# Kernel optimization log

Measured on AMD Instinct MI355X. Metric: run time of the kernel, lower is better.

The kernel has to match this reference:

```python
import jax, jax.numpy as jnp
import numpy as np

B, N_H, N_W, DIM, HEADS = 2, 64, 64, 768, 12
HINT = 1024
HIDDEN = DIM * 2       # LTRM expand_ratio = 2
K_ECA = 5              # ECA kernel for C=768: int(|log2(768)/2 + 0.5|)=5 (odd)
TH_LO, TH_HI, MIN_EDGE = 0.02, 0.98, 64


def setup_inputs() -> dict:
    key = jax.random.key(0)
    ks = jax.random.split(key, 12)
    N = N_H * N_W
    x = jax.random.normal(ks[0], (B, N, DIM), jnp.float32)
    # alpha hint: left half = uniform noise (uncertain -> edge tokens),
    # right half = binary blocks aligned to the 16px token cells (easy tokens)
    blocks = (jax.random.uniform(ks[1], (B, 1, N_H, N_W)) > 0.5).astype(jnp.float32)
    blocks_up = jnp.repeat(jnp.repeat(blocks, HINT // N_H, axis=2), HINT // N_W, axis=3)
    noise = jax.random.uniform(ks[2], (B, 1, HINT, HINT))
    col = jnp.arange(HINT)[None, None, None, :]
    alpha_hint = jnp.where(col < HINT // 2, noise, blocks_up)
    s = 0.02
    return {
        "x": x,
        "alpha_hint": alpha_hint,
        # global attention (Hiera-style patched MaskUnitAttention, q_stride=1)
        "qkv_w": jax.random.normal(ks[3], (DIM, 3 * DIM), jnp.float32) * s,
        "qkv_b": jnp.zeros((3 * DIM,), jnp.float32),
        "proj_w": jax.random.normal(ks[4], (DIM, DIM), jnp.float32) * s,
        "proj_b": jnp.zeros((DIM,), jnp.float32),
        # LTRM
        "ln_g": jnp.ones((DIM,), jnp.float32),
        "ln_b": jnp.zeros((DIM,), jnp.float32),
        "fc1_w": jax.random.normal(ks[5], (DIM, HIDDEN), jnp.float32) * s,
        "fc1_b": jnp.zeros((HIDDEN,), jnp.float32),
        "fc2_w": jax.random.normal(ks[6], (HIDDEN, DIM), jnp.float32) * s,  # zeros in ckpt; random for non-trivial math
        "fc2_b": jnp.zeros((DIM,), jnp.float32),
        "eca_w": jax.random.normal(ks[7], (K_ECA,), jnp.float32) * 0.2,
    }


def _edge_mask(alpha_hint):
    # F.interpolate(mode='area') with exact integer factor == block mean
    Bn = alpha_hint.shape[0]
    f_h, f_w = HINT // N_H, HINT // N_W
    hint = alpha_hint.reshape(Bn, N_H, f_h, N_W, f_w).mean(axis=(2, 4)).reshape(Bn, N_H * N_W)
    edge = (hint > TH_LO) & (hint < TH_HI)
    # per-batch fallback: too few edge tokens -> route everything to attention
    edge = jnp.where(edge.sum(axis=1, keepdims=True) < MIN_EDGE, True, edge)
    return edge  # [B, N] bool


def _layernorm(h, g, b, eps=1e-5):
    mu = h.mean(-1, keepdims=True)
    var = ((h - mu) ** 2).mean(-1, keepdims=True)
    return (h - mu) * jax.lax.rsqrt(var + eps) * g + b


def reference(x, alpha_hint, qkv_w, qkv_b, proj_w, proj_b,
              ln_g, ln_b, fc1_w, fc1_b, fc2_w, fc2_b, eca_w):
    Bn, N, C = x.shape
    hd = C // HEADS
    edge = _edge_mask(alpha_hint)                      # [B, N] bool

    # ---- edge path: global SDPA restricted to edge tokens (masked form of
    # the gather->attend->scatter routing: same math, edge keys only) ----
    qkv = (x @ qkv_w + qkv_b).reshape(Bn, N, 3, HEADS, hd)
    q = qkv[:, :, 0].transpose(0, 2, 1, 3)             # [B,H,N,hd]
    k = qkv[:, :, 1].transpose(0, 2, 1, 3)
    v = qkv[:, :, 2].transpose(0, 2, 1, 3)
    scores = jnp.einsum('bhqd,bhkd->bhqk', q, k) / jnp.sqrt(jnp.asarray(hd, x.dtype))
    scores = scores + jnp.where(edge[:, None, None, :], 0.0, -1e9).astype(x.dtype)
    attn = jax.nn.softmax(scores, axis=-1)
    o = jnp.einsum('bhqk,bhkd->bhqd', attn, v)
    o = o.transpose(0, 2, 1, 3).reshape(Bn, N, C)
    attn_out = x + (o @ proj_w + proj_b)               # residual around attention

    # ---- easy path: LTRM (subset of tokens -> DWConv branch skipped,
    # exactly as in LTRM.forward when N != H*W) ----
    h = _layernorm(x, ln_g, ln_b)
    h = jax.nn.gelu(h @ fc1_w + fc1_b, approximate=False)
    h = jax.nn.gelu(h, approximate=False)
    h = h @ fc2_w + fc2_b                              # [B,N,C]
    # ECA: avg-pool over the routed (easy) token set -> masked mean
    easy = ~edge
    cnt = jnp.maximum(easy.sum(axis=1).astype(x.dtype), 1.0)      # [B]
    pooled = (h * easy[..., None]).sum(axis=1) / cnt[:, None]     # [B,C]
    g = jax.lax.conv_general_dilated(
        pooled[:, None, :], eca_w.reshape(1, 1, K_ECA), (1,), 'SAME',
        dimension_numbers=('NCH', 'OIH', 'NCH'))[:, 0, :]          # [B,C]
    h = h * jax.nn.sigmoid(g)[:, None, :]
    ltrm_out = x + h

    # ---- scatter-combine ----
    return jnp.where(edge[..., None], attn_out, ltrm_out)
```

## Files before the change

kernel.cpp:

```cpp
#include <hip/hip_runtime.h>

using u16 = unsigned short;
using short8 = __attribute__((ext_vector_type(8))) short;
using f32x4 = __attribute__((ext_vector_type(4))) float;

#define NTOK 4096
#define CDIM 768
#define QKVD 2304
#define NHEAD 12
#define NSPLIT 4
#define SCALE2 0.18033688011112042f
#define THRRAW 44.3614195558f

__device__ __forceinline__ u16 f2bf(float f) {
  unsigned u = __float_as_uint(f);
  u += 0x7FFFu + ((u >> 16) & 1u);
  return (u16)(u >> 16);
}
__device__ __forceinline__ float bf2f(u16 v) {
  return __uint_as_float(((unsigned)v) << 16);
}
__device__ __forceinline__ float fast_exp2(float x) {
  float r;
  asm("v_exp_f32 %0, %1" : "=v"(r) : "v"(x));
  return r;
}
__device__ __forceinline__ unsigned cvtpk(float lo, float hi) {
  unsigned r;
  asm("v_cvt_pk_bf16_f32 %0, %1, %2" : "=v"(r) : "v"(lo), "v"(hi));
  return r;
}

__device__ __forceinline__ void gload_lds16(const void* g, void* l) {
  __builtin_amdgcn_global_load_lds(
      (__attribute__((address_space(1))) void*)g,
      (__attribute__((address_space(3))) void*)l, 16u, 0, 0u);
}

__device__ __forceinline__ float gelu_exact(float z) {
  return 0.5f * z * (1.0f + erff(z * 0.70710678118654752f));
}

__global__ __launch_bounds__(256) void pool_hint_kernel(
    const float* __restrict__ ah, float* __restrict__ hint)
{
  const int bid = blockIdx.x;
  const int b = bid >> 6, cr = bid & 63;
  const int t = threadIdx.x;
  const float* base = ah + ((size_t)b * 1024 + (size_t)cr * 16) * 1024;
  float s = 0.f;
#pragma unroll
  for (int pr = 0; pr < 16; ++pr) {
    float4 v = *(const float4*)(base + (size_t)pr * 1024 + t * 4);
    s += v.x + v.y + v.z + v.w;
  }
  s += __shfl_xor(s, 1);
  s += __shfl_xor(s, 2);
  if ((t & 3) == 0)
    hint[b * NTOK + cr * 64 + (t >> 2)] = s * (1.f / 256.f);
}

__global__ __launch_bounds__(1024) void finalize_edge_kernel(
    const float* __restrict__ hint, int* __restrict__ edge,
    int* __restrict__ qidx, int* __restrict__ eidx,
    int* __restrict__ cntE, int* __restrict__ cntZ)
{
  const int b = blockIdx.x, t = threadIdx.x;
  __shared__ int wsum[16];
  __shared__ int scntE, scntZ, stot;
  int bits[4]; int s = 0;
#pragma unroll
  for (int j = 0; j < 4; ++j) {
    float h = hint[b * NTOK + t * 4 + j];
    bits[j] = (h > 0.02f && h < 0.98f) ? 1 : 0;
    s += bits[j];
    qidx[b * NTOK + t * 4 + j] = -1;
    eidx[b * NTOK + t * 4 + j] = -1;
  }
  int sw = s;
#pragma unroll
  for (int d = 1; d < 64; d <<= 1) sw += __shfl_xor(sw, d);
  const int l = t & 63, w = t >> 6;
  if (l == 0) wsum[w] = sw;
  if (t == 0) { scntE = 0; scntZ = 0; }
  __syncthreads();
  if (t == 0) { int a = 0; for (int i = 0; i < 16; ++i) a += wsum[i]; stot = a; }
  __syncthreads();
  const bool fb = stot < 64;
#pragma unroll
  for (int j = 0; j < 4; ++j) {
    int e = fb ? 1 : bits[j];
    edge[b * NTOK + t * 4 + j] = e;
    if (e) {
      int p = atomicAdd(&scntE, 1);
      qidx[b * NTOK + p] = t * 4 + j;
    } else {
      int p = atomicAdd(&scntZ, 1);
      eidx[b * NTOK + p] = t * 4 + j;
    }
  }
  __syncthreads();
  if (t == 0) { cntE[b] = scntE; cntZ[b] = scntZ; }
}

__global__ __launch_bounds__(256) void ln_kernel(
    const float* __restrict__ x, const float* __restrict__ gam,
    const float* __restrict__ bet, u16* __restrict__ lnb, u16* __restrict__ xb)
{
  const int row = blockIdx.x, t = threadIdx.x;
  const float* xr = x + (size_t)row * CDIM;
  float v[3];
#pragma unroll
  for (int j = 0; j < 3; ++j) v[j] = xr[t + j * 256];
  float s = v[0] + v[1] + v[2];
  float ss = v[0] * v[0] + v[1] * v[1] + v[2] * v[2];
#pragma unroll
  for (int d = 1; d < 64; d <<= 1) { s += __shfl_xor(s, d); ss += __shfl_xor(ss, d); }
  __shared__ float red[8];
  const int l = t & 63, w = t >> 6;
  if (l == 0) { red[w * 2] = s; red[w * 2 + 1] = ss; }
  __syncthreads();
  s = red[0] + red[2] + red[4] + red[6];
  ss = red[1] + red[3] + red[5] + red[7];
  const float mu = s * (1.f / 768.f);
  const float rstd = rsqrtf(ss * (1.f / 768.f) - mu * mu + 1e-5f);
#pragma unroll
  for (int j = 0; j < 3; ++j) {
    const int cc = t + j * 256;
    lnb[(size_t)row * CDIM + cc] = f2bf((v[j] - mu) * rstd * gam[cc] + bet[cc]);
    xb[(size_t)row * CDIM + cc] = f2bf(v[j]);
  }
}

__global__ __launch_bounds__(256) void transpose_all_kernel(
    const float* __restrict__ qkv_w, const float* __restrict__ proj_w,
    const float* __restrict__ fc1_w, const float* __restrict__ fc2_w,
    u16* __restrict__ qkvT, u16* __restrict__ projT,
    u16* __restrict__ fc1T, u16* __restrict__ fc2T)
{
  __shared__ float tile[32][33];
  int bid = blockIdx.x;
  const float* in; u16* outp; int K, N, bx, by;
  if (bid < 1728)      { in = qkv_w;  outp = qkvT; K = 768;  N = 2304; bx = bid % 72; by = bid / 72; }
  else if (bid < 2304) { bid -= 1728; in = proj_w; outp = projT; K = 768;  N = 768;  bx = bid % 24; by = bid / 24; }
  else if (bid < 3456) { bid -= 2304; in = fc1_w;  outp = fc1T; K = 768;  N = 1536; bx = bid % 48; by = bid / 48; }
  else                 { bid -= 3456; in = fc2_w;  outp = fc2T; K = 1536; N = 768;  bx = bid % 24; by = bid / 24; }
  const int tx = threadIdx.x & 31, ty = threadIdx.x >> 5;
#pragma unroll
  for (int j = 0; j < 32; j += 8)
    tile[ty + j][tx] = in[(size_t)(by * 32 + ty + j) * N + bx * 32 + tx];
  __syncthreads();
#pragma unroll
  for (int j = 0; j < 32; j += 8)
    outp[(size_t)(bx * 32 + ty + j) * K + by * 32 + tx] = f2bf(tile[tx][ty + j]);
}

template <int EPI, bool GATHER_A, bool SCATTER_OUT>
__global__ __launch_bounds__(256) void gemm_bt(
    const u16* __restrict__ A, const u16* __restrict__ Bt,
    const float* __restrict__ bias, const float* __restrict__ resid,
    const int* __restrict__ list, void* __restrict__ outp, int N, int K)
{
  const int bm = blockIdx.x, bn = blockIdx.y;
  const int b = bm >> 5, bmi = bm & 31;
  const int rb = bmi * 128;
  if (list[b * NTOK + rb] < 0) return;

  __shared__ __align__(16) u16 lA[128 * 32];
  __shared__ __align__(16) u16 lB[128 * 32];
  const int t = threadIdx.x;
  const int l = t & 63, w = t >> 6;
  const int g = l >> 4, c = l & 15;
  const int wr = w >> 1, wc = w & 1;

  f32x4 acc[4][4];
#pragma unroll
  for (int i = 0; i < 4; ++i)
#pragma unroll
    for (int j = 0; j < 4; ++j) acc[i][j] = f32x4{0.f, 0.f, 0.f, 0.f};

  const int srow = t >> 2;
  const int sslot = (t & 3) ^ (srow & 3);
  int ta0, ta1;
  if constexpr (GATHER_A) {
    ta0 = list[b * NTOK + rb + srow];       if (ta0 < 0) ta0 = 0;
    ta1 = list[b * NTOK + rb + 64 + srow];  if (ta1 < 0) ta1 = 0;
  } else {
    ta0 = rb + srow;
    ta1 = rb + 64 + srow;
  }
  const u16* gA0 = A + ((size_t)b * NTOK + ta0) * K + sslot * 8;
  const u16* gA1 = A + ((size_t)b * NTOK + ta1) * K + sslot * 8;
  const u16* gB0 = Bt + (size_t)(bn * 128 + srow) * K + sslot * 8;
  const u16* gB1 = Bt + (size_t)(bn * 128 + 64 + srow) * K + sslot * 8;
  char* ldA = (char*)lA + w * 1024;
  char* ldB = (char*)lB + w * 1024;

  for (int k0 = 0; k0 < K; k0 += 32) {
    __syncthreads();
    gload_lds16(gA0 + k0, ldA);
    gload_lds16(gA1 + k0, ldA + 4096);
    gload_lds16(gB0 + k0, ldB);
    gload_lds16(gB1 + k0, ldB + 4096);
    __syncthreads();
    short8 af[4], bfr[4];
#pragma unroll
    for (int mi = 0; mi < 4; ++mi) {
      int row = wr * 64 + mi * 16 + c;
      af[mi] = *(const short8*)((const char*)lA + row * 64 + ((g ^ (row & 3)) << 4));
    }
#pragma unroll
    for (int ni = 0; ni < 4; ++ni) {
      int row = wc * 64 + ni * 16 + c;
      bfr[ni] = *(const short8*)((const char*)lB + row * 64 + ((g ^ (row & 3)) << 4));
    }
#pragma unroll
    for (int mi = 0; mi < 4; ++mi)
#pragma unroll
      for (int ni = 0; ni < 4; ++ni)
        acc[mi][ni] = __builtin_amdgcn_mfma_f32_16x16x32_bf16(af[mi], bfr[ni], acc[mi][ni], 0, 0, 0);
  }

#pragma unroll
  for (int mi = 0; mi < 4; ++mi) {
#pragma unroll
    for (int ni = 0; ni < 4; ++ni) {
      const int col = bn * 128 + wc * 64 + ni * 16 + c;
      const float bv = bias[col];
      const int prow0 = rb + wr * 64 + mi * 16 + g * 4;
#pragma unroll
      for (int r = 0; r < 4; ++r) {
        float v = acc[mi][ni][r] + bv;
        int orow;
        if constexpr (SCATTER_OUT) {
          int tok = list[b * NTOK + prow0 + r];
          if (tok < 0) continue;
          orow = tok;
        } else {
          orow = prow0 + r;
        }
        const size_t idx = ((size_t)b * NTOK + orow) * N + col;
        if constexpr (EPI == 0) {
          ((u16*)outp)[idx] = f2bf(v);
        } else if constexpr (EPI == 1) {
          ((float*)outp)[idx] = v + resid[idx];
        } else if constexpr (EPI == 2) {
          ((u16*)outp)[idx] = f2bf(gelu_exact(gelu_exact(v)));
        } else {
          ((float*)outp)[idx] = v;
        }
      }
    }
  }
}

__global__ __launch_bounds__(256) void flash_part_kernel(
    const u16* __restrict__ qkv, const int* __restrict__ cntE,
    u16* __restrict__ partO, float2* __restrict__ partML)
{
  const int qt = blockIdx.x;
  const int bh = blockIdx.y;
  const int sp = blockIdx.z;
  const int b = bh / NHEAD, h = bh % NHEAD;
  const int cnt = cntE[b];
  if (qt * 128 >= cnt) return;

  const int ntiles = (cnt + 63) >> 6;
  const int per = (ntiles + NSPLIT - 1) / NSPLIT;
  const int tA = sp * per;
  const int tB = min(ntiles, tA + per);
  if (tA >= tB) return;
  const int tBf = min(tB, cnt >> 6);
  const int rem = cnt & 63;

  __shared__ __align__(16) u16 lK[2][64 * 64];
  __shared__ __align__(16) u16 lV[2][64 * 64];
  __shared__ __align__(16) u16 lP[4][32 * 64];

  const int t = threadIdx.x;
  const int l = t & 63, w = t >> 6;
  const int g = l >> 4, c = l & 15;
  const int kp = t & 31, db = t >> 5;
  const size_t tokbase = (size_t)b * NTOK;

  short8 qf[2][2];
#pragma unroll
  for (int mi = 0; mi < 2; ++mi) {
    const int pos = qt * 128 + w * 32 + mi * 16 + c;
    const u16* qp = qkv + (tokbase + pos) * QKVD + h * 64;
#pragma unroll
    for (int kb = 0; kb < 2; ++kb)
      qf[mi][kb] = *(const short8*)(qp + kb * 32 + g * 8);
  }

  f32x4 oacc[2][4];
  float m2run[2], lrun[2];
#pragma unroll
  for (int mi = 0; mi < 2; ++mi) {
#pragma unroll
    for (int nd = 0; nd < 4; ++nd) oacc[mi][nd] = f32x4{0.f, 0.f, 0.f, 0.f};
    m2run[mi] = -1e30f; lrun[mi] = 0.f;
  }

  char* lPw = (char*)lP[w];

  auto stageK = [&](int kt, int buf) {
#pragma unroll
    for (int j = 0; j < 2; ++j) {
      int seg = j * 256 + t;
      int row = seg >> 3;
      int sl = (seg & 7) ^ (row & 7);
      gload_lds16(qkv + (tokbase + kt * 64 + row) * QKVD + CDIM + h * 64 + sl * 8,
                  (char*)lK[buf] + j * 4096 + w * 1024);
    }
  };
  uint4 va, vb;
  auto loadV = [&](int kt) {
    const u16* vg = qkv + (tokbase + kt * 64 + kp * 2) * QKVD + 2 * CDIM + h * 64 + db * 8;
    va = *(const uint4*)vg;
    vb = *(const uint4*)(vg + QKVD);
  };
  auto writeV = [&](int buf) {
    union { uint4 q; u16 s[8]; } u0, u1; u0.q = va; u1.q = vb;
    char* lvb = (char*)lV[buf];
#pragma unroll
    for (int j = 0; j < 8; ++j) {
      int d = db * 8 + j;
      unsigned pk = (unsigned)u0.s[j] | ((unsigned)u1.s[j] << 16);
      *(unsigned*)(lvb + d * 128 + ((kp * 4) ^ ((d & 7) << 4))) = pk;
    }
  };

  int cur = 0;
  stageK(tA, 0);
  loadV(tA);
  writeV(0);
  __syncthreads();

#define FLASH_TILE(MASKED)                                                        \
  {                                                                               \
    const bool hasNext = (kt + 1 < tB);                                           \
    if (hasNext) { stageK(kt + 1, cur ^ 1); loadV(kt + 1); }                      \
    const char* lKc = (const char*)lK[cur];                                       \
    short8 kf[4][2];                                                              \
    _Pragma("unroll")                                                             \
    for (int ni = 0; ni < 4; ++ni) {                                              \
      int row = ni * 16 + c;                                                      \
      _Pragma("unroll")                                                           \
      for (int kb = 0; kb < 2; ++kb)                                              \
        kf[ni][kb] = *(const short8*)(lKc + row * 128 +                           \
                                      (((kb * 4 + g) ^ (row & 7)) << 4));         \
    }                                                                             \
    f32x4 st[2][4];                                                               \
    __builtin_amdgcn_s_setprio(1);                                                \
    _Pragma("unroll")                                                             \
    for (int mi = 0; mi < 2; ++mi)                                                \
      _Pragma("unroll")                                                           \
      for (int ni = 0; ni < 4; ++ni) {                                            \
        f32x4 sv = f32x4{0.f, 0.f, 0.f, 0.f};                                     \
        sv = __builtin_amdgcn_mfma_f32_16x16x32_bf16(kf[ni][0], qf[mi][0], sv, 0, 0, 0); \
        sv = __builtin_amdgcn_mfma_f32_16x16x32_bf16(kf[ni][1], qf[mi][1], sv, 0, 0, 0); \
        st[mi][ni] = sv;                                                          \
      }                                                                           \
    __builtin_amdgcn_s_setprio(0);                                                \
    if (MASKED) {                                                                 \
      _Pragma("unroll")                                                           \
      for (int mi = 0; mi < 2; ++mi)                                              \
        _Pragma("unroll")                                                         \
        for (int ni = 0; ni < 4; ++ni)                                            \
          _Pragma("unroll")                                                       \
          for (int r = 0; r < 4; ++r)                                             \
            if (ni * 16 + g * 4 + r >= rem) st[mi][ni][r] = -1e30f;               \
    }                                                                             \
    _Pragma("unroll")                                                             \
    for (int mi = 0; mi < 2; ++mi) {                                              \
      float mx = fmaxf(                                                           \
          fmaxf(fmaxf(fmaxf(st[mi][0][0], st[mi][0][1]), fmaxf(st[mi][0][2], st[mi][0][3])), \
                fmaxf(fmaxf(st[mi][1][0], st[mi][1][1]), fmaxf(st[mi][1][2], st[mi][1][3]))), \
          fmaxf(fmaxf(fmaxf(st[mi][2][0], st[mi][2][1]), fmaxf(st[mi][2][2], st[mi][2][3])), \
                fmaxf(fmaxf(st[mi][3][0], st[mi][3][1]), fmaxf(st[mi][3][2], st[mi][3][3])))); \
      mx = fmaxf(mx, __shfl_xor(mx, 16));                                         \
      mx = fmaxf(mx, __shfl_xor(mx, 32));                                         \
      if (!__all(mx - m2run[mi] <= THRRAW)) {                                     \
        const float mnew = fmaxf(m2run[mi], mx);                                  \
        const float alpha = fast_exp2((m2run[mi] - mnew) * SCALE2);               \
        m2run[mi] = mnew;                                                         \
        lrun[mi] *= alpha;                                                        \
        _Pragma("unroll")                                                         \
        for (int nd = 0; nd < 4; ++nd)                                            \
          _Pragma("unroll")                                                       \
          for (int r = 0; r < 4; ++r) oacc[mi][nd][r] *= alpha;                   \
      }                                                                           \
      const float msc = m2run[mi] * SCALE2;                                       \
      float rs = 0.f;                                                             \
      const int qrow = mi * 16 + c;                                               \
      char* pbase = lPw + qrow * 128;                                             \
      const int swz = (qrow & 7) << 4;                                            \
      _Pragma("unroll")                                                           \
      for (int ni = 0; ni < 4; ++ni) {                                            \
        float p0 = fast_exp2(fmaf(st[mi][ni][0], SCALE2, -msc));                  \
        float p1 = fast_exp2(fmaf(st[mi][ni][1], SCALE2, -msc));                  \
        float p2 = fast_exp2(fmaf(st[mi][ni][2], SCALE2, -msc));                  \
        float p3 = fast_exp2(fmaf(st[mi][ni][3], SCALE2, -msc));                  \
        rs += (p0 + p1) + (p2 + p3);                                              \
        *(uint2*)(pbase + ((ni * 32 + g * 8) ^ swz)) =                            \
            make_uint2(cvtpk(p0, p1), cvtpk(p2, p3));                             \
      }                                                                           \
      rs += __shfl_xor(rs, 16);                                                   \
      rs += __shfl_xor(rs, 32);                                                   \
      lrun[mi] += rs;                                                             \
    }                                                                             \
    const char* lVc = (const char*)lV[cur];                                       \
    _Pragma("unroll")                                                             \
    for (int kb = 0; kb < 2; ++kb) {                                              \
      short8 pb[2], vf[4];                                                        \
      _Pragma("unroll")                                                           \
      for (int mi = 0; mi < 2; ++mi) {                                            \
        int qrow = mi * 16 + c;                                                   \
        pb[mi] = *(const short8*)(lPw + qrow * 128 +                              \
                                  ((kb * 64 + g * 16) ^ ((qrow & 7) << 4)));      \
      }                                                                           \
      _Pragma("unroll")                                                           \
      for (int nd = 0; nd < 4; ++nd) {                                            \
        int d = nd * 16 + c;                                                      \
        vf[nd] = *(const short8*)(lVc + d * 128 +                                 \
                                  (((kb * 4 + g) ^ (d & 7)) << 4));               \
      }                                                                           \
      __builtin_amdgcn_s_setprio(1);                                              \
      _Pragma("unroll")                                                           \
      for (int mi = 0; mi < 2; ++mi)                                              \
        _Pragma("unroll")                                                         \
        for (int nd = 0; nd < 4; ++nd)                                            \
          oacc[mi][nd] = __builtin_amdgcn_mfma_f32_16x16x32_bf16(vf[nd], pb[mi], oacc[mi][nd], 0, 0, 0); \
      __builtin_amdgcn_s_setprio(0);                                              \
    }                                                                             \
    if (hasNext) writeV(cur ^ 1);                                                 \
    __syncthreads();                                                              \
    cur ^= 1;                                                                     \
  }

  int kt = tA;
  for (; kt < tBf; ++kt) FLASH_TILE(0)
  for (; kt < tB; ++kt) FLASH_TILE(1)
#undef FLASH_TILE

  const size_t pobase = ((size_t)(sp * 2 + b) * NHEAD + h) * NTOK;
#pragma unroll
  for (int mi = 0; mi < 2; ++mi) {
    const int pos = qt * 128 + w * 32 + mi * 16 + c;
    if (pos < cnt) {
      u16* op = partO + (pobase + pos) * 64;
#pragma unroll
      for (int nd = 0; nd < 4; ++nd) {
        ushort4 pk4;
        pk4.x = f2bf(oacc[mi][nd][0]);
        pk4.y = f2bf(oacc[mi][nd][1]);
        pk4.z = f2bf(oacc[mi][nd][2]);
        pk4.w = f2bf(oacc[mi][nd][3]);
        *(ushort4*)(op + nd * 16 + g * 4) = pk4;
      }
      if (g == 0)
        partML[pobase + pos] = make_float2(m2run[mi] * SCALE2, lrun[mi]);
    }
  }
}

__global__ __launch_bounds__(256) void flash_merge_kernel(
    const u16* __restrict__ partO, const float2* __restrict__ partML,
    const int* __restrict__ cntE, u16* __restrict__ obf)
{
  const int bh = blockIdx.y;
  const int b = bh / NHEAD, h = bh % NHEAD;
  const int t = threadIdx.x;
  const int pos = blockIdx.x * 4 + (t >> 6);
  const int d = t & 63;
  const int cnt = cntE[b];
  if (pos >= cnt) return;
  const int ntiles = (cnt + 63) >> 6;
  const int per = (ntiles + NSPLIT - 1) / NSPLIT;

  float2 ml[NSPLIT];
  float M = -3e38f;
#pragma unroll
  for (int sp = 0; sp < NSPLIT; ++sp) {
    if (sp * per < ntiles) {
      ml[sp] = partML[((size_t)(sp * 2 + b) * NHEAD + h) * NTOK + pos];
      M = fmaxf(M, ml[sp].x);
    }
  }
  float L = 0.f, O = 0.f;
#pragma unroll
  for (int sp = 0; sp < NSPLIT; ++sp) {
    if (sp * per < ntiles) {
      const float e = fast_exp2(ml[sp].x - M);
      L += ml[sp].y * e;
      O += e * bf2f(partO[(((size_t)(sp * 2 + b) * NHEAD + h) * NTOK + pos) * 64 + d]);
    }
  }
  obf[((size_t)b * NTOK + pos) * CDIM + h * 64 + d] = f2bf(O / L);
}

__global__ __launch_bounds__(256) void pool_partial_kernel(
    const float* __restrict__ h2, const int* __restrict__ edge, float* __restrict__ pooled)
{
  const int bid = blockIdx.x;
  const int b = bid / 48, rm = bid % 48;
  const int cg = rm / 16, ts = rm % 16;
  const int ch = cg * 256 + threadIdx.x;
  float s = 0.f;
  for (int tok = ts * 256; tok < ts * 256 + 256; ++tok) {
    if (!edge[b * NTOK + tok])
      s += h2[((size_t)b * NTOK + tok) * CDIM + ch];
  }
  atomicAdd(&pooled[b * CDIM + ch], s);
}

__global__ void eca_kernel(const float* __restrict__ pooled, const float* __restrict__ w5,
                           const int* __restrict__ ecnt, float* __restrict__ gate)
{
  const int b = blockIdx.x, c = threadIdx.x;
  const float inv = 1.f / fmaxf((float)ecnt[b], 1.f);
  float a = 0.f;
#pragma unroll
  for (int j = 0; j < 5; ++j) {
    int i = c - 2 + j;
    if (i >= 0 && i < CDIM) a += w5[j] * pooled[b * CDIM + i];
  }
  a *= inv;
  gate[b * CDIM + c] = 1.f / (1.f + __expf(-a));
}

__global__ __launch_bounds__(256) void combine_kernel(
    const float* __restrict__ x, const float* __restrict__ attn,
    const float* __restrict__ h2, const float* __restrict__ gate,
    const int* __restrict__ edge, float* __restrict__ out)
{
  const size_t i = ((size_t)blockIdx.x * 256 + threadIdx.x) * 4;
  const int b = (int)(i / ((size_t)NTOK * CDIM));
  const size_t r = i % ((size_t)NTOK * CDIM);
  const int tok = (int)(r / CDIM);
  const int cc = (int)(r % CDIM);
  float4 ov;
  if (edge[b * NTOK + tok]) {
    ov = *(const float4*)(attn + i);
  } else {
    float4 xv = *(const float4*)(x + i);
    float4 hv = *(const float4*)(h2 + i);
    float4 gv = *(const float4*)(gate + b * CDIM + cc);
    ov.x = xv.x + hv.x * gv.x;
    ov.y = xv.y + hv.y * gv.y;
    ov.z = xv.z + hv.z * gv.z;
    ov.w = xv.w + hv.w * gv.w;
  }
  *(float4*)(out + i) = ov;
}

extern "C" void kernel_launch(void* const* d_in, const int* in_sizes, int n_in,
                              void* d_out, int out_size, void* d_ws, size_t ws_size,
                              hipStream_t stream) {
  const float* x      = (const float*)d_in[0];
  const float* ah     = (const float*)d_in[1];
  const float* qkv_w  = (const float*)d_in[2];
  const float* qkv_b  = (const float*)d_in[3];
  const float* proj_w = (const float*)d_in[4];
  const float* proj_b = (const float*)d_in[5];
  const float* ln_g   = (const float*)d_in[6];
  const float* ln_b   = (const float*)d_in[7];
  const float* fc1_w  = (const float*)d_in[8];
  const float* fc1_b  = (const float*)d_in[9];
  const float* fc2_w  = (const float*)d_in[10];
  const float* fc2_b  = (const float*)d_in[11];
  const float* eca_w  = (const float*)d_in[12];
  float* out = (float*)d_out;

  char* ws = (char*)d_ws;
  size_t off = 0;
  auto alloc = [&](size_t bytes) {
    char* p = ws + off;
    off += (bytes + 255) & ~(size_t)255;
    return p;
  };
  float* hint   = (float*)alloc((size_t)2 * NTOK * 4);
  int*   edge   = (int*)alloc((size_t)2 * NTOK * 4);
  int*   qidx   = (int*)alloc((size_t)2 * NTOK * 4);
  int*   eidx   = (int*)alloc((size_t)2 * NTOK * 4);
  int*   cntE   = (int*)alloc(256);
  int*   cntZ   = (int*)alloc(256);
  u16*   xbf    = (u16*)alloc((size_t)2 * NTOK * CDIM * 2);
  u16*   lnbf   = (u16*)alloc((size_t)2 * NTOK * CDIM * 2);
  u16*   qkvT   = (u16*)alloc((size_t)QKVD * CDIM * 2);
  u16*   projT  = (u16*)alloc((size_t)CDIM * CDIM * 2);
  u16*   fc1T   = (u16*)alloc((size_t)1536 * CDIM * 2);
  u16*   fc2T   = (u16*)alloc((size_t)CDIM * 1536 * 2);
  u16*   qkvb   = (u16*)alloc((size_t)2 * NTOK * QKVD * 2);
  u16*   obf    = (u16*)alloc((size_t)2 * NTOK * CDIM * 2);
  u16*   h1bf   = (u16*)alloc((size_t)2 * NTOK * 1536 * 2);
  float* h2     = (float*)alloc((size_t)2 * NTOK * CDIM * 4);
  float* attn   = (float*)alloc((size_t)2 * NTOK * CDIM * 4);
  float* pooled = (float*)alloc((size_t)2 * CDIM * 4);
  float* gate   = (float*)alloc((size_t)2 * CDIM * 4);
  u16*   partO  = (u16*)h1bf;
  float* partML = attn;

  pool_hint_kernel<<<dim3(128), 256, 0, stream>>>(ah, hint);
  finalize_edge_kernel<<<dim3(2), 1024, 0, stream>>>(hint, edge, qidx, eidx, cntE, cntZ);
  ln_kernel<<<dim3(8192), 256, 0, stream>>>(x, ln_g, ln_b, lnbf, xbf);
  transpose_all_kernel<<<dim3(4608), 256, 0, stream>>>(
      qkv_w, proj_w, fc1_w, fc2_w, qkvT, projT, fc1T, fc2T);

  gemm_bt<0, true, false><<<dim3(64, 18), 256, 0, stream>>>(
      xbf, qkvT, qkv_b, nullptr, qidx, qkvb, 2304, 768);
  flash_part_kernel<<<dim3(32, 24, NSPLIT), 256, 0, stream>>>(qkvb, cntE, partO, (float2*)partML);
  flash_merge_kernel<<<dim3(1024, 24), 256, 0, stream>>>(partO, (const float2*)partML, cntE, obf);
  gemm_bt<1, false, true><<<dim3(64, 6), 256, 0, stream>>>(
      obf, projT, proj_b, x, qidx, attn, 768, 768);
  gemm_bt<2, true, false><<<dim3(64, 12), 256, 0, stream>>>(
      lnbf, fc1T, fc1_b, nullptr, eidx, h1bf, 1536, 768);
  gemm_bt<3, false, true><<<dim3(64, 6), 256, 0, stream>>>(
      h1bf, fc2T, fc2_b, nullptr, eidx, h2, 768, 1536);

  hipMemsetAsync(pooled, 0, (size_t)2 * CDIM * 4, stream);
  pool_partial_kernel<<<dim3(96), 256, 0, stream>>>(h2, edge, pooled);
  eca_kernel<<<dim3(2), 768, 0, stream>>>(pooled, eca_w, cntZ, gate);
  combine_kernel<<<dim3(6144), 256, 0, stream>>>(x, attn, h2, gate, edge, out);
}
```

Before: 504.5 us.

## Restructure flash attention to single-wave blocks with register-resident K, narrow GEMM tiles

The flash partial kernel now runs one 64-thread wave per block on 32 queries. K fragments are loaded straight from global memory into registers, double-buffered across iterations, and V goes into a single LDS buffer with no block-level barriers. This removes the shared K staging and the __syncthreads, and launches four times as many blocks. In exchange, each wave re-reads K/V from global memory and lP/lV reuse relies on intra-wave ordering. Separately, the proj and fc2 GEMMs get a BN=64 template variant with twice the grid width, so the small-N GEMMs launch more blocks.

```diff
diff --git a/kernel.cpp b/kernel.cpp
--- a/kernel.cpp
+++ b/kernel.cpp
@@ -155,29 +155,30 @@
     outp[(size_t)(bx * 32 + ty + j) * K + by * 32 + tx] = f2bf(tile[tx][ty + j]);
 }
 
-template <int EPI, bool GATHER_A, bool SCATTER_OUT>
+template <int EPI, bool GATHER_A, bool SCATTER_OUT, int BN>
 __global__ __launch_bounds__(256) void gemm_bt(
     const u16* __restrict__ A, const u16* __restrict__ Bt,
     const float* __restrict__ bias, const float* __restrict__ resid,
     const int* __restrict__ list, void* __restrict__ outp, int N, int K)
 {
+  constexpr int NN = BN / 32;
   const int bm = blockIdx.x, bn = blockIdx.y;
   const int b = bm >> 5, bmi = bm & 31;
   const int rb = bmi * 128;
   if (list[b * NTOK + rb] < 0) return;
 
   __shared__ __align__(16) u16 lA[128 * 32];
-  __shared__ __align__(16) u16 lB[128 * 32];
+  __shared__ __align__(16) u16 lB[BN * 32];
   const int t = threadIdx.x;
   const int l = t & 63, w = t >> 6;
   const int g = l >> 4, c = l & 15;
   const int wr = w >> 1, wc = w & 1;
 
-  f32x4 acc[4][4];
+  f32x4 acc[4][NN];
 #pragma unroll
   for (int i = 0; i < 4; ++i)
 #pragma unroll
-    for (int j = 0; j < 4; ++j) acc[i][j] = f32x4{0.f, 0.f, 0.f, 0.f};
+    for (int j = 0; j < NN; ++j) acc[i][j] = f32x4{0.f, 0.f, 0.f, 0.f};
 
   const int srow = t >> 2;
   const int sslot = (t & 3) ^ (srow & 3);
@@ -191,8 +192,8 @@
   }
   const u16* gA0 = A + ((size_t)b * NTOK + ta0) * K + sslot * 8;
   const u16* gA1 = A + ((size_t)b * NTOK + ta1) * K + sslot * 8;
-  const u16* gB0 = Bt + (size_t)(bn * 128 + srow) * K + sslot * 8;
-  const u16* gB1 = Bt + (size_t)(bn * 128 + 64 + srow) * K + sslot * 8;
+  const u16* gB0 = Bt + (size_t)(bn * BN + srow) * K + sslot * 8;
+  const u16* gB1 = (BN == 128) ? Bt + (size_t)(bn * BN + 64 + srow) * K + sslot * 8 : nullptr;
   char* ldA = (char*)lA + w * 1024;
   char* ldB = (char*)lB + w * 1024;
 
@@ -201,31 +202,31 @@
     gload_lds16(gA0 + k0, ldA);
     gload_lds16(gA1 + k0, ldA + 4096);
     gload_lds16(gB0 + k0, ldB);
-    gload_lds16(gB1 + k0, ldB + 4096);
+    if constexpr (BN == 128) gload_lds16(gB1 + k0, ldB + 4096);
     __syncthreads();
-    short8 af[4], bfr[4];
+    short8 af[4], bfr[NN];
 #pragma unroll
     for (int mi = 0; mi < 4; ++mi) {
       int row = wr * 64 + mi * 16 + c;
       af[mi] = *(const short8*)((const char*)lA + row * 64 + ((g ^ (row & 3)) << 4));
     }
 #pragma unroll
-    for (int ni = 0; ni < 4; ++ni) {
-      int row = wc * 64 + ni * 16 + c;
+    for (int ni = 0; ni < NN; ++ni) {
+      int row = wc * (BN / 2) + ni * 16 + c;
       bfr[ni] = *(const short8*)((const char*)lB + row * 64 + ((g ^ (row & 3)) << 4));
     }
 #pragma unroll
     for (int mi = 0; mi < 4; ++mi)
 #pragma unroll
-      for (int ni = 0; ni < 4; ++ni)
+      for (int ni = 0; ni < NN; ++ni)
         acc[mi][ni] = __builtin_amdgcn_mfma_f32_16x16x32_bf16(af[mi], bfr[ni], acc[mi][ni], 0, 0, 0);
   }
 
 #pragma unroll
   for (int mi = 0; mi < 4; ++mi) {
 #pragma unroll
-    for (int ni = 0; ni < 4; ++ni) {
-      const int col = bn * 128 + wc * 64 + ni * 16 + c;
+    for (int ni = 0; ni < NN; ++ni) {
+      const int col = bn * BN + wc * (BN / 2) + ni * 16 + c;
       const float bv = bias[col];
       const int prow0 = rb + wr * 64 + mi * 16 + g * 4;
 #pragma unroll
@@ -254,7 +255,7 @@
   }
 }
 
-__global__ __launch_bounds__(256) void flash_part_kernel(
+__global__ __launch_bounds__(64) void flash_part_kernel(
     const u16* __restrict__ qkv, const int* __restrict__ cntE,
     u16* __restrict__ partO, float2* __restrict__ partML)
 {
@@ -263,30 +264,26 @@
   const int sp = blockIdx.z;
   const int b = bh / NHEAD, h = bh % NHEAD;
   const int cnt = cntE[b];
-  if (qt * 128 >= cnt) return;
+  if (qt * 32 >= cnt) return;
 
   const int ntiles = (cnt + 63) >> 6;
   const int per = (ntiles + NSPLIT - 1) / NSPLIT;
   const int tA = sp * per;
   const int tB = min(ntiles, tA + per);
   if (tA >= tB) return;
-  const int tBf = min(tB, cnt >> 6);
-  const int rem = cnt & 63;
-
-  __shared__ __align__(16) u16 lK[2][64 * 64];
-  __shared__ __align__(16) u16 lV[2][64 * 64];
-  __shared__ __align__(16) u16 lP[4][32 * 64];
-
-  const int t = threadIdx.x;
-  const int l = t & 63, w = t >> 6;
+
+  __shared__ __align__(16) u16 lV[64 * 64];
+  __shared__ __align__(16) u16 lP[32 * 64];
+
+  const int l = threadIdx.x;
   const int g = l >> 4, c = l & 15;
-  const int kp = t & 31, db = t >> 5;
+  const int kp = l & 31, dgr = (l >> 5) * 4;
   const size_t tokbase = (size_t)b * NTOK;
 
   short8 qf[2][2];
 #pragma unroll
   for (int mi = 0; mi < 2; ++mi) {
-    const int pos = qt * 128 + w * 32 + mi * 16 + c;
+    const int pos = qt * 32 + mi * 16 + c;
     const u16* qp = qkv + (tokbase + pos) * QKVD + h * 64;
 #pragma unroll
     for (int kb = 0; kb < 2; ++kb)
@@ -302,55 +299,33 @@
     m2run[mi] = -1e30f; lrun[mi] = 0.f;
   }
 
-  char* lPw = (char*)lP[w];
-
-  auto stageK = [&](int kt, int buf) {
-#pragma unroll
-    for (int j = 0; j < 2; ++j) {
-      int seg = j * 256 + t;
-      int row = seg >> 3;
-      int sl = (seg & 7) ^ (row & 7);
-      gload_lds16(qkv + (tokbase + kt * 64 + row) * QKVD + CDIM + h * 64 + sl * 8,
-                  (char*)lK[buf] + j * 4096 + w * 1024);
-    }
-  };
-  uint4 va, vb;
-  auto loadV = [&](int kt) {
-    const u16* vg = qkv + (tokbase + kt * 64 + kp * 2) * QKVD + 2 * CDIM + h * 64 + db * 8;
-    va = *(const uint4*)vg;
-    vb = *(const uint4*)(vg + QKVD);
-  };
-  auto writeV = [&](int buf) {
-    union { uint4 q; u16 s[8]; } u0, u1; u0.q = va; u1.q = vb;
-    char* lvb = (char*)lV[buf];
-#pragma unroll
-    for (int j = 0; j < 8; ++j) {
-      int d = db * 8 + j;
-      unsigned pk = (unsigned)u0.s[j] | ((unsigned)u1.s[j] << 16);
-      *(unsigned*)(lvb + d * 128 + ((kp * 4) ^ ((d & 7) << 4))) = pk;
-    }
-  };
-
-  int cur = 0;
-  stageK(tA, 0);
-  loadV(tA);
-  writeV(0);
-  __syncthreads();
-
-#define FLASH_TILE(MASKED)                                                        \
+  short8 kS0[4][2], kS1[4][2];
+
+#define LOADK(KS, kt)                                                             \
   {                                                                               \
-    const bool hasNext = (kt + 1 < tB);                                           \
-    if (hasNext) { stageK(kt + 1, cur ^ 1); loadV(kt + 1); }                      \
-    const char* lKc = (const char*)lK[cur];                                       \
-    short8 kf[4][2];                                                              \
-    _Pragma("unroll")                                                             \
-    for (int ni = 0; ni < 4; ++ni) {                                              \
-      int row = ni * 16 + c;                                                      \
+    const u16* kg = qkv + (tokbase + (kt) * 64 + c) * QKVD + CDIM + h * 64 + g * 8; \
+    _Pragma("unroll")                                                             \
+    for (int ni = 0; ni < 4; ++ni)                                                \
       _Pragma("unroll")                                                           \
       for (int kb = 0; kb < 2; ++kb)                                              \
-        kf[ni][kb] = *(const short8*)(lKc + row * 128 +                           \
-                                      (((kb * 4 + g) ^ (row & 7)) << 4));         \
+        KS[ni][kb] = *(const short8*)(kg + (size_t)(ni * 16) * QKVD + kb * 32);   \
+  }
+
+#define FLASH_BODY(KS, kt)                                                        \
+  {                                                                               \
+    const bool msk = ((kt) * 64 + 64 > cnt);                                      \
+    const int rem = cnt - (kt) * 64;                                              \
+                   \
+    uint4 vv[8];                                                                  \
+    {                                                                             \
+      const u16* vg = qkv + (tokbase + (kt) * 64 + kp * 2) * QKVD + 2 * CDIM + h * 64 + dgr * 8; \
+      _Pragma("unroll")                                                           \
+      for (int dbb = 0; dbb < 4; ++dbb) {                                         \
+        vv[dbb]     = *(const uint4*)(vg + dbb * 8);                              \
+        vv[4 + dbb] = *(const uint4*)(vg + QKVD + dbb * 8);                       \
+      }                                                                           \
     }                                                                             \
+                                                       \
     f32x4 st[2][4];                                                               \
     __builtin_amdgcn_s_setprio(1);                                                \
     _Pragma("unroll")                                                             \
@@ -358,12 +333,12 @@
       _Pragma("unroll")                                                           \
       for (int ni = 0; ni < 4; ++ni) {                                            \
         f32x4 sv = f32x4{0.f, 0.f, 0.f, 0.f};                                     \
-        sv = __builtin_amdgcn_mfma_f32_16x16x32_bf16(kf[ni][0], qf[mi][0], sv, 0, 0, 0); \
-        sv = __builtin_amdgcn_mfma_f32_16x16x32_bf16(kf[ni][1], qf[mi][1], sv, 0, 0, 0); \
+        sv = __builtin_amdgcn_mfma_f32_16x16x32_bf16(KS[ni][0], qf[mi][0], sv, 0, 0, 0); \
+        sv = __builtin_amdgcn_mfma_f32_16x16x32_bf16(KS[ni][1], qf[mi][1], sv, 0, 0, 0); \
         st[mi][ni] = sv;                                                          \
       }                                                                           \
     __builtin_amdgcn_s_setprio(0);                                                \
-    if (MASKED) {                                                                 \
+    if (msk) {                                                                    \
       _Pragma("unroll")                                                           \
       for (int mi = 0; mi < 2; ++mi)                                              \
         _Pragma("unroll")                                                         \
@@ -372,17 +347,23 @@
           for (int r = 0; r < 4; ++r)                                             \
             if (ni * 16 + g * 4 + r >= rem) st[mi][ni][r] = -1e30f;               \
     }                                                                             \
-    _Pragma("unroll")                                                             \
-    for (int mi = 0; mi < 2; ++mi) {                                              \
-      float mx = fmaxf(                                                           \
+               \
+    float mx[2];                                                                  \
+    _Pragma("unroll")                                                             \
+    for (int mi = 0; mi < 2; ++mi)                                                \
+      mx[mi] = fmaxf(                                                             \
           fmaxf(fmaxf(fmaxf(st[mi][0][0], st[mi][0][1]), fmaxf(st[mi][0][2], st[mi][0][3])), \
                 fmaxf(fmaxf(st[mi][1][0], st[mi][1][1]), fmaxf(st[mi][1][2], st[mi][1][3]))), \
           fmaxf(fmaxf(fmaxf(st[mi][2][0], st[mi][2][1]), fmaxf(st[mi][2][2], st[mi][2][3])), \
                 fmaxf(fmaxf(st[mi][3][0], st[mi][3][1]), fmaxf(st[mi][3][2], st[mi][3][3])))); \
-      mx = fmaxf(mx, __shfl_xor(mx, 16));                                         \
-      mx = fmaxf(mx, __shfl_xor(mx, 32));                                         \
-      if (!__all(mx - m2run[mi] <= THRRAW)) {                                     \
-        const float mnew = fmaxf(m2run[mi], mx);                                  \
+    _Pragma("unroll")                                                             \
+    for (int mi = 0; mi < 2; ++mi) mx[mi] = fmaxf(mx[mi], __shfl_xor(mx[mi], 16));\
+    _Pragma("unroll")                                                             \
+    for (int mi = 0; mi < 2; ++mi) mx[mi] = fmaxf(mx[mi], __shfl_xor(mx[mi], 32));\
+    _Pragma("unroll")                                                             \
+    for (int mi = 0; mi < 2; ++mi) {                                              \
+      if (!__all(mx[mi] - m2run[mi] <= THRRAW)) {                                 \
+        const float mnew = fmaxf(m2run[mi], mx[mi]);                              \
         const float alpha = fast_exp2((m2run[mi] - mnew) * SCALE2);               \
         m2run[mi] = mnew;                                                         \
         lrun[mi] *= alpha;                                                        \
@@ -391,10 +372,14 @@
           _Pragma("unroll")                                                       \
           for (int r = 0; r < 4; ++r) oacc[mi][nd][r] *= alpha;                   \
       }                                                                           \
+    }                                                                             \
+    float rs[2];                                                                  \
+    _Pragma("unroll")                                                             \
+    for (int mi = 0; mi < 2; ++mi) {                                              \
       const float msc = m2run[mi] * SCALE2;                                       \
-      float rs = 0.f;                                                             \
+      float a = 0.f;                                                              \
       const int qrow = mi * 16 + c;                                               \
-      char* pbase = lPw + qrow * 128;                                             \
+      char* pbase = (char*)lP + qrow * 128;                                       \
       const int swz = (qrow & 7) << 4;                                            \
       _Pragma("unroll")                                                           \
       for (int ni = 0; ni < 4; ++ni) {                                            \
@@ -402,28 +387,45 @@
         float p1 = fast_exp2(fmaf(st[mi][ni][1], SCALE2, -msc));                  \
         float p2 = fast_exp2(fmaf(st[mi][ni][2], SCALE2, -msc));                  \
         float p3 = fast_exp2(fmaf(st[mi][ni][3], SCALE2, -msc));                  \
-        rs += (p0 + p1) + (p2 + p3);                                              \
+        a += (p0 + p1) + (p2 + p3);                                               \
         *(uint2*)(pbase + ((ni * 32 + g * 8) ^ swz)) =                            \
             make_uint2(cvtpk(p0, p1), cvtpk(p2, p3));                             \
       }                                                                           \
-      rs += __shfl_xor(rs, 16);                                                   \
-      rs += __shfl_xor(rs, 32);                                                   \
-      lrun[mi] += rs;                                                             \
+      rs[mi] = a;                                                                 \
     }                                                                             \
-    const char* lVc = (const char*)lV[cur];                                       \
+    _Pragma("unroll")                                                             \
+    for (int mi = 0; mi < 2; ++mi) rs[mi] += __shfl_xor(rs[mi], 16);              \
+    _Pragma("unroll")                                                             \
+    for (int mi = 0; mi < 2; ++mi) rs[mi] += __shfl_xor(rs[mi], 32);              \
+    _Pragma("unroll")                                                             \
+    for (int mi = 0; mi < 2; ++mi) lrun[mi] += rs[mi];                            \
+                 \
+    _Pragma("unroll")                                                             \
+    for (int dbb = 0; dbb < 4; ++dbb) {                                           \
+      union { uint4 q; u16 s[8]; } u0, u1;                                        \
+      u0.q = vv[dbb]; u1.q = vv[4 + dbb];                                         \
+      const int dd0 = (dgr + dbb) * 8;                                            \
+      _Pragma("unroll")                                                           \
+      for (int j = 0; j < 8; ++j) {                                               \
+        int d = dd0 + j;                                                          \
+        *(unsigned*)((char*)lV + d * 128 + ((kp * 4) ^ ((d & 7) << 4))) =         \
+            (unsigned)u0.s[j] | ((unsigned)u1.s[j] << 16);                        \
+      }                                                                           \
+    }                                                                             \
+                                                    \
     _Pragma("unroll")                                                             \
     for (int kb = 0; kb < 2; ++kb) {                                              \
       short8 pb[2], vf[4];                                                        \
       _Pragma("unroll")                                                           \
       for (int mi = 0; mi < 2; ++mi) {                                            \
         int qrow = mi * 16 + c;                                                   \
-        pb[mi] = *(const short8*)(lPw + qrow * 128 +                              \
+        pb[mi] = *(const short8*)((char*)lP + qrow * 128 +                        \
                                   ((kb * 64 + g * 16) ^ ((qrow & 7) << 4)));      \
       }                                                                           \
       _Pragma("unroll")                                                           \
       for (int nd = 0; nd < 4; ++nd) {                                            \
         int d = nd * 16 + c;                                                      \
-        vf[nd] = *(const short8*)(lVc + d * 128 +                                 \
+        vf[nd] = *(const short8*)((char*)lV + d * 128 +                           \
                                   (((kb * 4 + g) ^ (d & 7)) << 4));               \
       }                                                                           \
       __builtin_amdgcn_s_setprio(1);                                              \
@@ -434,20 +436,25 @@
           oacc[mi][nd] = __builtin_amdgcn_mfma_f32_16x16x32_bf16(vf[nd], pb[mi], oacc[mi][nd], 0, 0, 0); \
       __builtin_amdgcn_s_setprio(0);                                              \
     }                                                                             \
-    if (hasNext) writeV(cur ^ 1);                                                 \
-    __syncthreads();                                                              \
-    cur ^= 1;                                                                     \
-  }
-
+  }
+
+  LOADK(kS0, tA);
   int kt = tA;
-  for (; kt < tBf; ++kt) FLASH_TILE(0)
-  for (; kt < tB; ++kt) FLASH_TILE(1)
-#undef FLASH_TILE
+  while (true) {
+    if (kt + 1 < tB) LOADK(kS1, kt + 1);
+    FLASH_BODY(kS0, kt)
+    if (++kt >= tB) break;
+    if (kt + 1 < tB) LOADK(kS0, kt + 1);
+    FLASH_BODY(kS1, kt)
+    if (++kt >= tB) break;
+  }
+#undef FLASH_BODY
+#undef LOADK
 
   const size_t pobase = ((size_t)(sp * 2 + b) * NHEAD + h) * NTOK;
 #pragma unroll
   for (int mi = 0; mi < 2; ++mi) {
-    const int pos = qt * 128 + w * 32 + mi * 16 + c;
+    const int pos = qt * 32 + mi * 16 + c;
     if (pos < cnt) {
       u16* op = partO + (pobase + pos) * 64;
 #pragma unroll
@@ -608,15 +615,15 @@
   transpose_all_kernel<<<dim3(4608), 256, 0, stream>>>(
       qkv_w, proj_w, fc1_w, fc2_w, qkvT, projT, fc1T, fc2T);
 
-  gemm_bt<0, true, false><<<dim3(64, 18), 256, 0, stream>>>(
+  gemm_bt<0, true, false, 128><<<dim3(64, 18), 256, 0, stream>>>(
       xbf, qkvT, qkv_b, nullptr, qidx, qkvb, 2304, 768);
-  flash_part_kernel<<<dim3(32, 24, NSPLIT), 256, 0, stream>>>(qkvb, cntE, partO, (float2*)partML);
+  flash_part_kernel<<<dim3(128, 24, NSPLIT), 64, 0, stream>>>(qkvb, cntE, partO, (float2*)partML);
   flash_merge_kernel<<<dim3(1024, 24), 256, 0, stream>>>(partO, (const float2*)partML, cntE, obf);
-  gemm_bt<1, false, true><<<dim3(64, 6), 256, 0, stream>>>(
+  gemm_bt<1, false, true, 64><<<dim3(64, 12), 256, 0, stream>>>(
       obf, projT, proj_b, x, qidx, attn, 768, 768);
-  gemm_bt<2, true, false><<<dim3(64, 12), 256, 0, stream>>>(
+  gemm_bt<2, true, false, 128><<<dim3(64, 12), 256, 0, stream>>>(
       lnbf, fc1T, fc1_b, nullptr, eidx, h1bf, 1536, 768);
-  gemm_bt<3, false, true><<<dim3(64, 6), 256, 0, stream>>>(
+  gemm_bt<3, false, true, 64><<<dim3(64, 12), 256, 0, stream>>>(
       h1bf, fc2T, fc2_b, nullptr, eidx, h2, 768, 1536);
 
   hipMemsetAsync(pooled, 0, (size_t)2 * CDIM * 4, stream);
```

New measurement: 461.8 us. -8.5%, faster.
